# Kernel optimization log

Measured on AMD Instinct MI355X. Metric: run time of the kernel, lower is better.

## Reference

```python
import jax, jax.numpy as jnp
import numpy as np

B, T, D, H, C = 128, 1000, 40, 128, 8  # batch, time, input feats, hidden, classes


def _lstm_layer(x, Wih, Whh, bih, bhh):
    """Unidirectional LSTM over time. x: [B,T,Din] -> [B,T,H]. PyTorch gate order i,f,g,o."""
    Bn = x.shape[0]
    Hn = Whh.shape[1]
    b = bih + bhh
    def step(carry, xt):
        h, c = carry
        g = xt @ Wih.T + h @ Whh.T + b  # [B,4H]
        i, f, gg, o = jnp.split(g, 4, axis=-1)
        c = jax.nn.sigmoid(f) * c + jax.nn.sigmoid(i) * jnp.tanh(gg)
        h = jax.nn.sigmoid(o) * jnp.tanh(c)
        return (h, c), h
    h0 = jnp.zeros((Bn, Hn), x.dtype)
    _, hs = jax.lax.scan(step, (h0, h0), jnp.swapaxes(x, 0, 1))  # scan over time
    return jnp.swapaxes(hs, 0, 1)


def _bilstm_layer(x, pf, pb):
    fwd = _lstm_layer(x, *pf)
    bwd = jnp.flip(_lstm_layer(jnp.flip(x, 1), *pb), 1)
    return jnp.concatenate([fwd, bwd], axis=-1)  # [B,T,2H]


def setup_inputs() -> dict:
    key = jax.random.key(0)
    ks = jax.random.split(key, 16)
    s = 0.05
    def rn(k, shape):
        return jax.random.normal(k, shape, jnp.float32) * s
    inp = {"x": jax.random.normal(ks[0], (B, T, D), jnp.float32)}
    inp["ln_g"] = jnp.ones((D,), jnp.float32)
    inp["ln_b"] = jnp.zeros((D,), jnp.float32)
    dims = [D, 2 * H]  # layer-0 input feats, layer-1 input feats
    i = 1
    for l in range(2):
        for d in ("f", "b"):
            inp[f"Wih_{d}{l}"] = rn(ks[i], (4 * H, dims[l])); i += 1
            inp[f"Whh_{d}{l}"] = rn(ks[i], (4 * H, H)); i += 1
            inp[f"bih_{d}{l}"] = jnp.zeros((4 * H,), jnp.float32)
            inp[f"bhh_{d}{l}"] = jnp.zeros((4 * H,), jnp.float32)
    inp["attn_W1"] = rn(ks[i], (H, 2 * H)); i += 1
    inp["attn_b1"] = jnp.zeros((H,), jnp.float32)
    inp["attn_w2"] = rn(ks[i], (1, H)); i += 1
    inp["fc_W1"] = rn(ks[i], (H, 2 * H)); i += 1
    inp["fc_b1"] = jnp.zeros((H,), jnp.float32)
    inp["fc_W2"] = rn(ks[i], (C, H)); i += 1
    inp["fc_b2"] = jnp.zeros((C,), jnp.float32)
    return inp


def reference(x, ln_g, ln_b,
              Wih_f0, Whh_f0, bih_f0, bhh_f0, Wih_b0, Whh_b0, bih_b0, bhh_b0,
              Wih_f1, Whh_f1, bih_f1, bhh_f1, Wih_b1, Whh_b1, bih_b1, bhh_b1,
              attn_W1, attn_b1, attn_w2, fc_W1, fc_b1, fc_W2, fc_b2):
    # LayerNorm over feature dim (eps=1e-5, PyTorch default)
    mu = jnp.mean(x, axis=-1, keepdims=True)
    var = jnp.var(x, axis=-1, keepdims=True)
    xn = (x - mu) * jax.lax.rsqrt(var + 1e-5) * ln_g + ln_b
    # 2-layer bidirectional LSTM
    h = _bilstm_layer(xn, (Wih_f0, Whh_f0, bih_f0, bhh_f0), (Wih_b0, Whh_b0, bih_b0, bhh_b0))
    h = _bilstm_layer(h, (Wih_f1, Whh_f1, bih_f1, bhh_f1), (Wih_b1, Whh_b1, bih_b1, bhh_b1))
    # attention pooling: Linear-Tanh-Linear(no bias) -> softmax over time
    scores = jnp.tanh(h @ attn_W1.T + attn_b1) @ attn_w2[0]  # [B,T]
    w = jax.nn.softmax(scores, axis=1)
    ctx = jnp.einsum('bt,btd->bd', w, h)  # [B,2H]
    # MLP classifier head
    hid = jax.nn.relu(ctx @ fc_W1.T + fc_b1)
    return hid @ fc_W2.T + fc_b2  # [B,C] logits
```

## Files before the change

### kernel.cpp

```cpp
#include <hip/hip_runtime.h>
#include <hip/hip_fp16.h>

#define T_ 1000

typedef float v2f __attribute__((ext_vector_type(2)));
typedef __fp16 h2t __attribute__((ext_vector_type(2)));
typedef __fp16 h8v_t __attribute__((ext_vector_type(8)));

#if defined(__has_builtin)
#if __has_builtin(__builtin_amdgcn_fdot2)
#define HAS_FDOT2 1
#endif
#endif
#ifndef HAS_FDOT2
#define HAS_FDOT2 0
#endif

#define REC_BARRIER() asm volatile("s_waitcnt lgkmcnt(0)\n\ts_barrier" ::: "memory")

__device__ __forceinline__ float sigf(float x) { return 1.0f / (1.0f + __expf(-x)); }
__device__ __forceinline__ float tanh_fast(float x) { return 1.0f - 2.0f / (1.0f + __expf(2.0f * x)); }
__device__ __forceinline__ float dot4(float4 a, float4 b) {
  return a.x * b.x + a.y * b.y + a.z * b.z + a.w * b.w;
}
__device__ __forceinline__ void pkfma(v2f& acc, float4 w, float4 v) {
  v2f wl; wl[0] = w.x; wl[1] = w.y;
  v2f wh; wh[0] = w.z; wh[1] = w.w;
  v2f vl; vl[0] = v.x; vl[1] = v.y;
  v2f vh; vh[0] = v.z; vh[1] = v.w;
  acc += wl * vl;
  acc += wh * vh;
}
__device__ __forceinline__ unsigned short f2bf(float f) {
  unsigned u = __float_as_uint(f);
  u = (u + 0x7fffu + ((u >> 16) & 1u)) >> 16;
  return (unsigned short)u;
}
__device__ __forceinline__ float bf2f(unsigned short h) {
  return __uint_as_float(((unsigned)h) << 16);
}
__device__ __forceinline__ float4 bf4_to_f4(ushort4 u) {
  float4 r;
  r.x = bf2f(u.x); r.y = bf2f(u.y); r.z = bf2f(u.z); r.w = bf2f(u.w);
  return r;
}

__global__ void bail_kernel(float* out, int n) {
  for (int i = threadIdx.x; i < n; i += 256) out[i] = 0.0f;
}

__global__ __launch_bounds__(256) void ln_stats_kernel(const float* __restrict__ x,
                                                       float* __restrict__ mu_arr,
                                                       float* __restrict__ rs_arr) {
  const int lane = threadIdx.x & 63;
  const int w = threadIdx.x >> 6;
  const long row = (long)blockIdx.x * 4 + w;
  float v = (lane < 40) ? x[row * 40 + lane] : 0.0f;
  float s1 = v, s2 = v * v;
  for (int m = 32; m; m >>= 1) {
    s1 += __shfl_xor(s1, m, 64);
    s2 += __shfl_xor(s2, m, 64);
  }
  if (lane == 0) {
    const float mu = s1 * (1.0f / 40.0f);
    const float var = s2 * (1.0f / 40.0f) - mu * mu;
    mu_arr[row] = mu;
    rs_arr[row] = rsqrtf(var + 1e-5f);
  }
}

__global__ __launch_bounds__(256, 2) void gemm_xw0(
    const float* __restrict__ x,
    const float* __restrict__ mu_arr, const float* __restrict__ rs_arr,
    const float* __restrict__ ln_g, const float* __restrict__ ln_b,
    const float* __restrict__ Wf, const float* __restrict__ Wb,
    __fp16* __restrict__ xwf, __fp16* __restrict__ xwb,
    int Tc, int t0f, int t0b) {
  __shared__ float As[64 * 44];
  __shared__ float Bs[128 * 44];
  const int tid = threadIdx.x;
  const int tx = tid & 15, ty = tid >> 4;
  const int r0 = blockIdx.x * 64;
  const int jt = blockIdx.y;
  const int dir = jt >> 2, nh = jt & 3;
  const float* __restrict__ W = dir ? Wb : Wf;
  __fp16* __restrict__ out = dir ? xwb : xwf;
  const int jbase = nh * 128;
  const int t0 = dir ? t0b : t0f;

  float4* As4 = (float4*)As;
  float4* Bs4 = (float4*)Bs;
  {
    const int row = tid >> 2;
    const int t4 = tid & 3;
    const int r = r0 + row;
    const int br = r / Tc;
    const long xrow = (long)br * T_ + t0 + (r - br * Tc);
    const float mu = mu_arr[xrow];
    const float rs = rs_arr[xrow];
#pragma unroll
    for (int m = 0; m < 3; ++m) {
      const int k4 = t4 + m * 4;
      if (k4 < 10) {
        const float4 v = *(const float4*)&x[xrow * 40 + k4 * 4];
        const float4 g4 = *(const float4*)&ln_g[k4 * 4];
        const float4 b4 = *(const float4*)&ln_b[k4 * 4];
        float4 xn;
        xn.x = (v.x - mu) * rs * g4.x + b4.x;
        xn.y = (v.y - mu) * rs * g4.y + b4.y;
        xn.z = (v.z - mu) * rs * g4.z + b4.z;
        xn.w = (v.w - mu) * rs * g4.w + b4.w;
        As4[row * 11 + k4] = xn;
      }
    }
  }
  {
    const int row = tid & 127;
    const int h = tid >> 7;
#pragma unroll
    for (int m = 0; m < 5; ++m) {
      const int k4 = h + m * 2;
      Bs4[row * 11 + k4] = *(const float4*)&W[(long)(jbase + row) * 40 + k4 * 4];
    }
  }
  __syncthreads();

  v2f acc2[4][8];
#pragma unroll
  for (int r = 0; r < 4; ++r)
#pragma unroll
    for (int c2 = 0; c2 < 8; ++c2) acc2[r][c2] = 0.0f;
#pragma unroll 1
  for (int k4 = 0; k4 < 10; ++k4) {
    float4 av[4];
#pragma unroll
    for (int r = 0; r < 4; ++r) av[r] = As4[(ty * 4 + r) * 11 + k4];
#pragma unroll
    for (int c2 = 0; c2 < 8; ++c2) {
      const float4 bv = Bs4[(tx + 16 * c2) * 11 + k4];
#pragma unroll
      for (int r = 0; r < 4; ++r) pkfma(acc2[r][c2], av[r], bv);
    }
  }
#pragma unroll
  for (int r = 0; r < 4; ++r) {
    const long ob = (long)(r0 + ty * 4 + r) * 512 + jbase + tx;
#pragma unroll
    for (int c2 = 0; c2 < 8; ++c2) out[ob + c2 * 16] = (__fp16)(acc2[r][c2][0] + acc2[r][c2][1]);
  }
}

__global__ __launch_bounds__(512) void rec_fused(
    const __fp16* __restrict__ xw_f, const __fp16* __restrict__ xw_b,
    const float* __restrict__ Whh_f, const float* __restrict__ Whh_b,
    const float* __restrict__ bih_f, const float* __restrict__ bhh_f,
    const float* __restrict__ bih_b, const float* __restrict__ bhh_b,
    float* __restrict__ h0out, unsigned short* __restrict__ h1out, int out_bf16,
    float* __restrict__ state, int Tc, int t0f, int t0b, int first) {
  const int tid = threadIdx.x;
  const int u = (tid >> 6) * 16 + ((tid & 63) >> 2);
  const int p = tid & 3;
  const int brow = blockIdx.x & 127;
  const int dir = blockIdx.x >> 7;
  const __fp16* __restrict__ xw = dir ? xw_b : xw_f;
  const float* __restrict__ Whh = dir ? Whh_b : Whh_f;
  const float* __restrict__ bih = dir ? bih_b : bih_f;
  const float* __restrict__ bhh = dir ? bhh_b : bhh_f;
  const int t0 = dir ? t0b : t0f;

  h2t whp[4][16];
#pragma unroll
  for (int g = 0; g < 4; ++g) {
    const float4* wr4 = (const float4*)(Whh + (g * 128 + u) * 128);
#pragma unroll
    for (int ff = 0; ff < 4; ++ff) {
      const int c4 = (ff + p) & 3;
      const float4 wa = wr4[p * 8 + c4 * 2];
      const float4 wb = wr4[p * 8 + c4 * 2 + 1];
      h2t t0v; t0v[0] = (__fp16)wa.x; t0v[1] = (__fp16)wa.y;
      h2t t1v; t1v[0] = (__fp16)wa.z; t1v[1] = (__fp16)wa.w;
      h2t t2v; t2v[0] = (__fp16)wb.x; t2v[1] = (__fp16)wb.y;
      h2t t3v; t3v[0] = (__fp16)wb.z; t3v[1] = (__fp16)wb.w;
      whp[g][ff * 4 + 0] = t0v;
      whp[g][ff * 4 + 1] = t1v;
      whp[g][ff * 4 + 2] = t2v;
      whp[g][ff * 4 + 3] = t3v;
    }
  }
  const int myrow = p * 128 + u;
  const float bias_p = bih[myrow] + bhh[myrow];

  __shared__ h2t h16[2][64];
  __shared__ float hring[2][8][128];
  float* sblk = state + (long)blockIdx.x * 256;
  float c = 0.0f, hlast = 0.0f;
  if (first) {
    if (tid < 64) { h2t z; z[0] = (__fp16)0.0f; z[1] = (__fp16)0.0f; h16[0][tid] = z; }
  } else {
    if (tid < 64) {
      h2t pr; pr[0] = (__fp16)sblk[2 * tid]; pr[1] = (__fp16)sblk[2 * tid + 1];
      h16[0][tid] = pr;
    }
    c = sblk[128 + u];
  }
  const long gbase = (long)brow * Tc;
  float xr[8];
#pragma unroll
  for (int v = 0; v < 8; ++v) {
    xr[v] = 0.0f;
    if (v < Tc) {
      const int tr = dir ? (Tc - 1 - v) : v;
      xr[v] = (float)xw[(gbase + tr) * 512 + myrow];
    }
  }
  __syncthreads();

  const int nSB = (Tc + 7) / 8;
  const long obase = (long)brow * T_;
  for (int sb = 0; sb < nSB; ++sb) {
    const int rb = sb & 1;
#pragma unroll
    for (int su = 0; su < 8; ++su) {
      const int s = sb * 8 + su;
      if (s >= Tc) break;
      const int rdq = su & 1, wrq = rdq ^ 1;
      if (su == 0 && sb > 0) {
#pragma unroll
        for (int e = 0; e < 2; ++e) {
          const int idx = tid + e * 512;
          const int v = idx >> 7, j = idx & 127;
          const int s2 = (sb - 1) * 8 + v;
          const int tt = dir ? (Tc - 1 - s2) : s2;
          const long oidx = (obase + (t0 + tt)) * 256 + dir * 128 + j;
          const float hval = hring[rb ^ 1][v][j];
          if (out_bf16) h1out[oidx] = f2bf(hval);
          else          h0out[oidx] = hval;
        }
      }
      float a0 = 0.f, a1 = 0.f, a2 = 0.f, a3 = 0.f;
      const h8v_t* hp = (const h8v_t*)h16[rdq];
#pragma unroll
      for (int ff = 0; ff < 4; ++ff) {
        const int c4 = (ff + p) & 3;
        const h8v_t hx = hp[p * 4 + c4];
        const h2t x0 = __builtin_shufflevector(hx, hx, 0, 1);
        const h2t x1 = __builtin_shufflevector(hx, hx, 2, 3);
        const h2t x2 = __builtin_shufflevector(hx, hx, 4, 5);
        const h2t x3 = __builtin_shufflevector(hx, hx, 6, 7);
#if HAS_FDOT2
        a0 = __builtin_amdgcn_fdot2(x0, whp[0][ff * 4 + 0], a0, false);
        a0 = __builtin_amdgcn_fdot2(x1, whp[0][ff * 4 + 1], a0, false);
        a0 = __builtin_amdgcn_fdot2(x2, whp[0][ff * 4 + 2], a0, false);
        a0 = __builtin_amdgcn_fdot2(x3, whp[0][ff * 4 + 3], a0, false);
        a1 = __builtin_amdgcn_fdot2(x0, whp[1][ff * 4 + 0], a1, false);
        a1 = __builtin_amdgcn_fdot2(x1, whp[1][ff * 4 + 1], a1, false);
        a1 = __builtin_amdgcn_fdot2(x2, whp[1][ff * 4 + 2], a1, false);
        a1 = __builtin_amdgcn_fdot2(x3, whp[1][ff * 4 + 3], a1, false);
        a2 = __builtin_amdgcn_fdot2(x0, whp[2][ff * 4 + 0], a2, false);
        a2 = __builtin_amdgcn_fdot2(x1, whp[2][ff * 4 + 1], a2, false);
        a2 = __builtin_amdgcn_fdot2(x2, whp[2][ff * 4 + 2], a2, false);
        a2 = __builtin_amdgcn_fdot2(x3, whp[2][ff * 4 + 3], a2, false);
        a3 = __builtin_amdgcn_fdot2(x0, whp[3][ff * 4 + 0], a3, false);
        a3 = __builtin_amdgcn_fdot2(x1, whp[3][ff * 4 + 1], a3, false);
        a3 = __builtin_amdgcn_fdot2(x2, whp[3][ff * 4 + 2], a3, false);
        a3 = __builtin_amdgcn_fdot2(x3, whp[3][ff * 4 + 3], a3, false);
#else
        const h2t xs[4] = {x0, x1, x2, x3};
#pragma unroll
        for (int j = 0; j < 4; ++j) {
          a0 = fmaf((float)xs[j][0], (float)whp[0][ff * 4 + j][0], a0);
          a0 = fmaf((float)xs[j][1], (float)whp[0][ff * 4 + j][1], a0);
          a1 = fmaf((float)xs[j][0], (float)whp[1][ff * 4 + j][0], a1);
          a1 = fmaf((float)xs[j][1], (float)whp[1][ff * 4 + j][1], a1);
          a2 = fmaf((float)xs[j][0], (float)whp[2][ff * 4 + j][0], a2);
          a2 = fmaf((float)xs[j][1], (float)whp[2][ff * 4 + j][1], a2);
          a3 = fmaf((float)xs[j][0], (float)whp[3][ff * 4 + j][0], a3);
          a3 = fmaf((float)xs[j][1], (float)whp[3][ff * 4 + j][1], a3);
        }
#endif
      }
      const float xin = xr[su] + bias_p;
      float pg0 = a0 + ((p == 0) ? xin : 0.0f);
      float pg1 = a1 + ((p == 1) ? xin : 0.0f);
      float pg2 = a2 + ((p == 2) ? xin : 0.0f);
      float pg3 = a3 + ((p == 3) ? xin : 0.0f);
      pg0 += __shfl_xor(pg0, 1, 64); pg0 += __shfl_xor(pg0, 2, 64);
      pg1 += __shfl_xor(pg1, 1, 64); pg1 += __shfl_xor(pg1, 2, 64);
      pg2 += __shfl_xor(pg2, 1, 64); pg2 += __shfl_xor(pg2, 2, 64);
      pg3 += __shfl_xor(pg3, 1, 64); pg3 += __shfl_xor(pg3, 2, 64);
      const float ig = sigf(pg0);
      const float fg = sigf(pg1);
      const float gg = tanh_fast(pg2);
      const float og = sigf(pg3);
      c = fg * c + ig * gg;
      const float hv2 = og * tanh_fast(c);
      if (p == 0) {
        ((__fp16*)h16[wrq])[u] = (__fp16)hv2;
        hring[rb][su][u] = hv2;
        hlast = hv2;
      }
      if (su == 7) {
#pragma unroll
        for (int v = 0; v < 8; ++v) {
          const int sn = s + 1 + v;
          xr[v] = 0.0f;
          if (sn < Tc) {
            const int tr = dir ? (Tc - 1 - sn) : sn;
            xr[v] = (float)xw[(gbase + tr) * 512 + myrow];
          }
        }
      }
      REC_BARRIER();
    }
  }
  {
    const int sbL = (Tc - 1) >> 3;
    const int cnt = Tc - sbL * 8;
    const int rbL = sbL & 1;
#pragma unroll
    for (int e = 0; e < 2; ++e) {
      const int idx = tid + e * 512;
      const int v = idx >> 7, j = idx & 127;
      if (v < cnt) {
        const int s2 = sbL * 8 + v;
        const int tt = dir ? (Tc - 1 - s2) : s2;
        const long oidx = (obase + (t0 + tt)) * 256 + dir * 128 + j;
        const float hval = hring[rbL][v][j];
        if (out_bf16) h1out[oidx] = f2bf(hval);
        else          h0out[oidx] = hval;
      }
    }
  }
  if (p == 0) { sblk[u] = hlast; sblk[128 + u] = c; }
}

__global__ __launch_bounds__(256, 2) void gemm_xw1(
    const float* __restrict__ h0,
    const float* __restrict__ Wf, const float* __restrict__ Wb,
    __fp16* __restrict__ xwf, __fp16* __restrict__ xwb,
    int Tc, int t0f, int t0b) {
  __shared__ float As[64 * 36];
  __shared__ float Bs[128 * 36];
  __shared__ int rowbase[64];
  const int tid = threadIdx.x;
  const int tx = tid & 15, ty = tid >> 4;
  const int r0 = blockIdx.x * 64;
  const int jt = blockIdx.y;
  const int dir = jt >> 2;
  const int nh = jt & 3;
  const float* __restrict__ W = dir ? Wb : Wf;
  __fp16* __restrict__ out = dir ? xwb : xwf;
  const int jbase = nh * 128;
  const int t0 = dir ? t0b : t0f;

  if (tid < 64) {
    const int r = r0 + tid;
    const int br = r / Tc;
    rowbase[tid] = br * T_ + t0 + (r - br * Tc);
  }

  float4* As4 = (float4*)As;
  float4* Bs4 = (float4*)Bs;
  v2f acc2[4][8];
#pragma unroll
  for (int r = 0; r < 4; ++r)
#pragma unroll
    for (int c2 = 0; c2 < 8; ++c2) acc2[r][c2] = 0.0f;
#pragma unroll 1
  for (int kk = 0; kk < 8; ++kk) {
    __syncthreads();
#pragma unroll
    for (int i = 0; i < 2; ++i) {
      const int q = tid + i * 256;
      const int row = q >> 3, k4 = q & 7;
      As4[row * 9 + k4] = *(const float4*)&h0[(long)rowbase[row] * 256 + kk * 32 + k4 * 4];
    }
#pragma unroll
    for (int i = 0; i < 4; ++i) {
      const int q = tid + i * 256;
      const int row = q >> 3, k4 = q & 7;
      Bs4[row * 9 + k4] = *(const float4*)&W[(long)(jbase + row) * 256 + kk * 32 + k4 * 4];
    }
    __syncthreads();
#pragma unroll 1
    for (int k4 = 0; k4 < 8; ++k4) {
      float4 av[4];
#pragma unroll
      for (int r = 0; r < 4; ++r) av[r] = As4[(ty * 4 + r) * 9 + k4];
#pragma unroll
      for (int c2 = 0; c2 < 8; ++c2) {
        const float4 bv = Bs4[(tx + 16 * c2) * 9 + k4];
#pragma unroll
        for (int r = 0; r < 4; ++r) pkfma(acc2[r][c2], av[r], bv);
      }
    }
  }
#pragma unroll
  for (int r = 0; r < 4; ++r) {
    const long ob = (long)(r0 + ty * 4 + r) * 512 + jbase + tx;
#pragma unroll
    for (int c2 = 0; c2 < 8; ++c2) out[ob + c2 * 16] = (__fp16)(acc2[r][c2][0] + acc2[r][c2][1]);
  }
}

__global__ __launch_bounds__(256, 2) void score_kernel(
    const unsigned short* __restrict__ h1b, const float* __restrict__ W1,
    const float* __restrict__ b1, const float* __restrict__ w2,
    float* __restrict__ scores) {
  __shared__ float As[64 * 36];
  __shared__ float Bs[128 * 36];
  const int tid = threadIdx.x;
  const int tx = tid & 15, ty = tid >> 4;
  const long r0 = (long)blockIdx.x * 64;

  float4* As4 = (float4*)As;
  float4* Bs4 = (float4*)Bs;
  v2f acc2[4][8];
#pragma unroll
  for (int r = 0; r < 4; ++r)
#pragma unroll
    for (int c2 = 0; c2 < 8; ++c2) acc2[r][c2] = 0.0f;
#pragma unroll 1
  for (int kk = 0; kk < 8; ++kk) {
    __syncthreads();
#pragma unroll
    for (int i = 0; i < 2; ++i) {
      const int q = tid + i * 256;
      const int row = q >> 3, k4 = q & 7;
      const ushort4 uv = *(const ushort4*)&h1b[(r0 + row) * 256 + kk * 32 + k4 * 4];
      As4[row * 9 + k4] = bf4_to_f4(uv);
    }
#pragma unroll
    for (int i = 0; i < 4; ++i) {
      const int q = tid + i * 256;
      const int row = q >> 3, k4 = q & 7;
      Bs4[row * 9 + k4] = *(const float4*)&W1[(long)row * 256 + kk * 32 + k4 * 4];
    }
    __syncthreads();
#pragma unroll 1
    for (int k4 = 0; k4 < 8; ++k4) {
      float4 av[4];
#pragma unroll
      for (int r = 0; r < 4; ++r) av[r] = As4[(ty * 4 + r) * 9 + k4];
#pragma unroll
      for (int c2 = 0; c2 < 8; ++c2) {
        const float4 bv = Bs4[(tx + 16 * c2) * 9 + k4];
#pragma unroll
        for (int r = 0; r < 4; ++r) pkfma(acc2[r][c2], av[r], bv);
      }
    }
  }
#pragma unroll
  for (int r = 0; r < 4; ++r) {
    float s = 0.0f;
#pragma unroll
    for (int c2 = 0; c2 < 8; ++c2) {
      const int col = tx + 16 * c2;
      s += tanh_fast(acc2[r][c2][0] + acc2[r][c2][1] + b1[col]) * w2[col];
    }
#pragma unroll
    for (int m = 1; m < 16; m <<= 1) s += __shfl_xor(s, m, 16);
    if (tx == 0) scores[r0 + ty * 4 + r] = s;
  }
}

__global__ __launch_bounds__(256, 2) void head_kernel(
    const float* __restrict__ scores, const unsigned short* __restrict__ h1b,
    const float* __restrict__ fW1, const float* __restrict__ fb1,
    const float* __restrict__ fW2, const float* __restrict__ fb2,
    float* __restrict__ outp) {
  const int b = blockIdx.x, tid = threadIdx.x;
  __shared__ float wls[1000];
  __shared__ float red[8];
  __shared__ __align__(16) float ctx[256];
  __shared__ __align__(16) float hid[128];

  float sv[4];
  float mx = -1e30f;
#pragma unroll
  for (int i = 0; i < 4; ++i) {
    const int t = tid + i * 256;
    sv[i] = (t < 1000) ? scores[b * 1000 + t] : -1e30f;
    mx = fmaxf(mx, sv[i]);
  }
  for (int m = 32; m; m >>= 1) mx = fmaxf(mx, __shfl_xor(mx, m, 64));
  if ((tid & 63) == 0) red[tid >> 6] = mx;
  __syncthreads();
  mx = fmaxf(fmaxf(red[0], red[1]), fmaxf(red[2], red[3]));
  float se = 0.0f;
#pragma unroll
  for (int i = 0; i < 4; ++i) {
    const int t = tid + i * 256;
    if (t < 1000) {
      const float e = __expf(sv[i] - mx);
      wls[t] = e;
      se += e;
    }
  }
  for (int m = 32; m; m >>= 1) se += __shfl_xor(se, m, 64);
  if ((tid & 63) == 0) red[4 + (tid >> 6)] = se;
  __syncthreads();
  const float rinv = 1.0f / (red[4] + red[5] + red[6] + red[7]);

  float a = 0.0f;
  const unsigned short* hb = h1b + (long)b * T_ * 256 + tid;
  for (int t = 0; t < T_; ++t) a = fmaf(wls[t], bf2f(hb[t * 256]), a);
  ctx[tid] = a * rinv;
  __syncthreads();
  if (tid < 128) {
    float s = fb1[tid];
    const float4* wr = (const float4*)&fW1[tid * 256];
    const float4* cc = (const float4*)ctx;
#pragma unroll
    for (int f = 0; f < 64; ++f) s += dot4(wr[f], cc[f]);
    hid[tid] = fmaxf(s, 0.0f);
  }
  __syncthreads();
  if (tid < 8) {
    float s = fb2[tid];
    const float4* wr = (const float4*)&fW2[tid * 128];
    const float4* hh = (const float4*)hid;
#pragma unroll
    for (int f = 0; f < 32; ++f) s += dot4(wr[f], hh[f]);
    outp[b * 8 + tid] = s;
  }
}

extern "C" void kernel_launch(void* const* d_in, const int* in_sizes, int n_in,
                              void* d_out, int out_size, void* d_ws, size_t ws_size,
                              hipStream_t stream) {
  (void)in_sizes; (void)n_in; (void)out_size;
  const float* x       = (const float*)d_in[0];
  const float* ln_g    = (const float*)d_in[1];
  const float* ln_b    = (const float*)d_in[2];
  const float* Wih_f0  = (const float*)d_in[3];
  const float* Whh_f0  = (const float*)d_in[4];
  const float* bih_f0  = (const float*)d_in[5];
  const float* bhh_f0  = (const float*)d_in[6];
  const float* Wih_b0  = (const float*)d_in[7];
  const float* Whh_b0  = (const float*)d_in[8];
  const float* bih_b0  = (const float*)d_in[9];
  const float* bhh_b0  = (const float*)d_in[10];
  const float* Wih_f1  = (const float*)d_in[11];
  const float* Whh_f1  = (const float*)d_in[12];
  const float* bih_f1  = (const float*)d_in[13];
  const float* bhh_f1  = (const float*)d_in[14];
  const float* Wih_b1  = (const float*)d_in[15];
  const float* Whh_b1  = (const float*)d_in[16];
  const float* bih_b1  = (const float*)d_in[17];
  const float* bhh_b1  = (const float*)d_in[18];
  const float* attn_W1 = (const float*)d_in[19];
  const float* attn_b1 = (const float*)d_in[20];
  const float* attn_w2 = (const float*)d_in[21];
  const float* fc_W1   = (const float*)d_in[22];
  const float* fc_b1   = (const float*)d_in[23];
  const float* fc_W2   = (const float*)d_in[24];
  const float* fc_b2   = (const float*)d_in[25];

  char* base = (char*)d_ws;
  size_t off = 0;
  auto alloc = [&](size_t bytes) {
    char* ptr = base + off;
    off += (bytes + 255) & ~(size_t)255;
    return ptr;
  };
  float*          h0    = (float*)alloc(32768000ull * 4);
  unsigned short* h1b   = (unsigned short*)alloc(32768000ull * 2);
  float*          state = (float*)alloc(65536ull * 4);
  float*          scor  = (float*)alloc(128000ull * 4);
  float*          mu_a  = (float*)alloc(128000ull * 4);
  float*          rs_a  = (float*)alloc(128000ull * 4);

  const size_t rem = (ws_size > off) ? (ws_size - off) : 0;
  static const int cands[16] = {1000, 500, 250, 200, 125, 100, 50, 40, 25, 20, 10, 8, 5, 4, 2, 1};
  int Tc = 0;
  for (int ci = 0; ci < 16; ++ci) {
    if (262144ull * (size_t)cands[ci] <= rem) { Tc = cands[ci]; break; }
  }
  if (Tc == 0) {
    bail_kernel<<<dim3(1), dim3(256), 0, stream>>>((float*)d_out, 1024);
    return;
  }
  __fp16* xwf = (__fp16*)(base + off);
  __fp16* xwb = xwf + 65536L * Tc;

  ln_stats_kernel<<<dim3(32000), dim3(256), 0, stream>>>(x, mu_a, rs_a);
  const int nch = T_ / Tc;
  for (int ch = 0; ch < nch; ++ch) {
    const int t0f = ch * Tc;
    const int t0b = T_ - (ch + 1) * Tc;
    gemm_xw0<<<dim3(2 * Tc, 8), dim3(256), 0, stream>>>(x, mu_a, rs_a, ln_g, ln_b,
                                                        Wih_f0, Wih_b0, xwf, xwb, Tc, t0f, t0b);
    rec_fused<<<dim3(256), dim3(512), 0, stream>>>(xwf, xwb, Whh_f0, Whh_b0,
                                                   bih_f0, bhh_f0, bih_b0, bhh_b0,
                                                   h0, h1b, 0, state, Tc, t0f, t0b,
                                                   (ch == 0) ? 1 : 0);
  }
  for (int ch = 0; ch < nch; ++ch) {
    const int t0f = ch * Tc;
    const int t0b = T_ - (ch + 1) * Tc;
    gemm_xw1<<<dim3(2 * Tc, 8), dim3(256), 0, stream>>>(h0, Wih_f1, Wih_b1, xwf, xwb, Tc, t0f, t0b);
    rec_fused<<<dim3(256), dim3(512), 0, stream>>>(xwf, xwb, Whh_f1, Whh_b1,
                                                   bih_f1, bhh_f1, bih_b1, bhh_b1,
                                                   h0, h1b, 1, state, Tc, t0f, t0b,
                                                   (ch == 0) ? 1 : 0);
  }
  score_kernel<<<dim3(2000), dim3(256), 0, stream>>>(h1b, attn_W1, attn_b1, attn_w2, scor);
  head_kernel<<<dim3(128), dim3(256), 0, stream>>>(scor, h1b, fc_W1, fc_b1, fc_W2, fc_b2,
                                                   (float*)d_out);
}
```

Baseline: 3.380 ms.

## Batch 8 rows per block and compute recurrent matvec with MFMA

```diff
diff --git a/kernel.cpp b/kernel.cpp
--- a/kernel.cpp
+++ b/kernel.cpp
@@ -6,15 +6,7 @@
 typedef float v2f __attribute__((ext_vector_type(2)));
 typedef __fp16 h2t __attribute__((ext_vector_type(2)));
 typedef __fp16 h8v_t __attribute__((ext_vector_type(8)));
-
-#if defined(__has_builtin)
-#if __has_builtin(__builtin_amdgcn_fdot2)
-#define HAS_FDOT2 1
-#endif
-#endif
-#ifndef HAS_FDOT2
-#define HAS_FDOT2 0
-#endif
+typedef float f32x4 __attribute__((ext_vector_type(4)));
 
 #define REC_BARRIER() asm volatile("s_waitcnt lgkmcnt(0)\n\ts_barrier" ::: "memory")
 
@@ -150,7 +142,7 @@
   }
 }
 
-__global__ __launch_bounds__(512) void rec_fused(
+__global__ __launch_bounds__(512) void rec_mfma(
     const __fp16* __restrict__ xw_f, const __fp16* __restrict__ xw_b,
     const float* __restrict__ Whh_f, const float* __restrict__ Whh_b,
     const float* __restrict__ bih_f, const float* __restrict__ bhh_f,
@@ -158,180 +150,130 @@
     float* __restrict__ h0out, unsigned short* __restrict__ h1out, int out_bf16,
     float* __restrict__ state, int Tc, int t0f, int t0b, int first) {
   const int tid = threadIdx.x;
-  const int u = (tid >> 6) * 16 + ((tid & 63) >> 2);
-  const int p = tid & 3;
-  const int brow = blockIdx.x & 127;
-  const int dir = blockIdx.x >> 7;
+  const int w = tid >> 6;
+  const int l = tid & 63;
+  const int al = l & 15;
+  const int kg = l >> 4;
+  const int dir = blockIdx.x & 1;
+  const int bg = blockIdx.x >> 1;
+  const int brow0 = bg * 8;
   const __fp16* __restrict__ xw = dir ? xw_b : xw_f;
   const float* __restrict__ Whh = dir ? Whh_b : Whh_f;
   const float* __restrict__ bih = dir ? bih_b : bih_f;
   const float* __restrict__ bhh = dir ? bhh_b : bhh_f;
   const int t0 = dir ? t0b : t0f;
 
-  h2t whp[4][16];
-#pragma unroll
-  for (int g = 0; g < 4; ++g) {
-    const float4* wr4 = (const float4*)(Whh + (g * 128 + u) * 128);
-#pragma unroll
-    for (int ff = 0; ff < 4; ++ff) {
-      const int c4 = (ff + p) & 3;
-      const float4 wa = wr4[p * 8 + c4 * 2];
-      const float4 wb = wr4[p * 8 + c4 * 2 + 1];
-      h2t t0v; t0v[0] = (__fp16)wa.x; t0v[1] = (__fp16)wa.y;
-      h2t t1v; t1v[0] = (__fp16)wa.z; t1v[1] = (__fp16)wa.w;
-      h2t t2v; t2v[0] = (__fp16)wb.x; t2v[1] = (__fp16)wb.y;
-      h2t t3v; t3v[0] = (__fp16)wb.z; t3v[1] = (__fp16)wb.w;
-      whp[g][ff * 4 + 0] = t0v;
-      whp[g][ff * 4 + 1] = t1v;
-      whp[g][ff * 4 + 2] = t2v;
-      whp[g][ff * 4 + 3] = t3v;
-    }
-  }
-  const int myrow = p * 128 + u;
-  const float bias_p = bih[myrow] + bhh[myrow];
-
-  __shared__ h2t h16[2][64];
-  __shared__ float hring[2][8][128];
-  float* sblk = state + (long)blockIdx.x * 256;
-  float c = 0.0f, hlast = 0.0f;
-  if (first) {
-    if (tid < 64) { h2t z; z[0] = (__fp16)0.0f; z[1] = (__fp16)0.0f; h16[0][tid] = z; }
-  } else {
-    if (tid < 64) {
-      h2t pr; pr[0] = (__fp16)sblk[2 * tid]; pr[1] = (__fp16)sblk[2 * tid + 1];
-      h16[0][tid] = pr;
-    }
-    c = sblk[128 + u];
-  }
-  const long gbase = (long)brow * Tc;
-  float xr[8];
-#pragma unroll
-  for (int v = 0; v < 8; ++v) {
-    xr[v] = 0.0f;
-    if (v < Tc) {
-      const int tr = dir ? (Tc - 1 - v) : v;
-      xr[v] = (float)xw[(gbase + tr) * 512 + myrow];
-    }
-  }
-  __syncthreads();
-
-  const int nSB = (Tc + 7) / 8;
-  const long obase = (long)brow * T_;
-  for (int sb = 0; sb < nSB; ++sb) {
-    const int rb = sb & 1;
-#pragma unroll
-    for (int su = 0; su < 8; ++su) {
-      const int s = sb * 8 + su;
-      if (s >= Tc) break;
-      const int rdq = su & 1, wrq = rdq ^ 1;
-      if (su == 0 && sb > 0) {
-#pragma unroll
-        for (int e = 0; e < 2; ++e) {
-          const int idx = tid + e * 512;
-          const int v = idx >> 7, j = idx & 127;
-          const int s2 = (sb - 1) * 8 + v;
-          const int tt = dir ? (Tc - 1 - s2) : s2;
-          const long oidx = (obase + (t0 + tt)) * 256 + dir * 128 + j;
-          const float hval = hring[rb ^ 1][v][j];
-          if (out_bf16) h1out[oidx] = f2bf(hval);
-          else          h0out[oidx] = hval;
-        }
+  h8v_t wA[4][4];
+#pragma unroll
+  for (int mt = 0; mt < 4; ++mt) {
+    const int grow = w * 64 + mt * 16 + al;
+#pragma unroll
+    for (int kt = 0; kt < 4; ++kt) {
+      const int k0 = kt * 32 + kg * 8;
+      const float4 wa = *(const float4*)&Whh[(long)grow * 128 + k0];
+      const float4 wb = *(const float4*)&Whh[(long)grow * 128 + k0 + 4];
+      h8v_t v;
+      v[0] = (__fp16)wa.x; v[1] = (__fp16)wa.y; v[2] = (__fp16)wa.z; v[3] = (__fp16)wa.w;
+      v[4] = (__fp16)wb.x; v[5] = (__fp16)wb.y; v[6] = (__fp16)wb.z; v[7] = (__fp16)wb.w;
+      wA[mt][kt] = v;
+    }
+  }
+  const int u2 = tid & 127;
+  const int q = tid >> 7;
+  float bsum[4];
+#pragma unroll
+  for (int g = 0; g < 4; ++g) bsum[g] = bih[g * 128 + u2] + bhh[g * 128 + u2];
+
+  __shared__ __align__(16) __fp16 h16[2][16][136];
+  __shared__ float gacc[512][9];
+
+  float* sblk = state + (long)blockIdx.x * 2048;
+  for (int i = tid; i < 2 * 16 * 136; i += 512) ((__fp16*)h16)[i] = (__fp16)0.0f;
+  float cc0 = 0.0f, cc1 = 0.0f;
+  __syncthreads();
+  if (!first) {
+    for (int i = tid; i < 1024; i += 512) {
+      const int b = i >> 7, uu = i & 127;
+      h16[0][b][(((uu >> 5) + b) & 3) * 32 + (uu & 31)] = (__fp16)sblk[i];
+    }
+    cc0 = sblk[1024 + (2 * q) * 128 + u2];
+    cc1 = sblk[1024 + (2 * q + 1) * 128 + u2];
+  }
+  float xwreg[8];
+  {
+    const int tr0 = dir ? (Tc - 1) : 0;
+#pragma unroll
+    for (int g = 0; g < 4; ++g)
+#pragma unroll
+      for (int j = 0; j < 2; ++j) {
+        const int b = 2 * q + j;
+        xwreg[g * 2 + j] = (float)xw[((long)(brow0 + b) * Tc + tr0) * 512 + g * 128 + u2];
       }
-      float a0 = 0.f, a1 = 0.f, a2 = 0.f, a3 = 0.f;
-      const h8v_t* hp = (const h8v_t*)h16[rdq];
-#pragma unroll
-      for (int ff = 0; ff < 4; ++ff) {
-        const int c4 = (ff + p) & 3;
-        const h8v_t hx = hp[p * 4 + c4];
-        const h2t x0 = __builtin_shufflevector(hx, hx, 0, 1);
-        const h2t x1 = __builtin_shufflevector(hx, hx, 2, 3);
-        const h2t x2 = __builtin_shufflevector(hx, hx, 4, 5);
-        const h2t x3 = __builtin_shufflevector(hx, hx, 6, 7);
-#if HAS_FDOT2
-        a0 = __builtin_amdgcn_fdot2(x0, whp[0][ff * 4 + 0], a0, false);
-        a0 = __builtin_amdgcn_fdot2(x1, whp[0][ff * 4 + 1], a0, false);
-        a0 = __builtin_amdgcn_fdot2(x2, whp[0][ff * 4 + 2], a0, false);
-        a0 = __builtin_amdgcn_fdot2(x3, whp[0][ff * 4 + 3], a0, false);
-        a1 = __builtin_amdgcn_fdot2(x0, whp[1][ff * 4 + 0], a1, false);
-        a1 = __builtin_amdgcn_fdot2(x1, whp[1][ff * 4 + 1], a1, false);
-        a1 = __builtin_amdgcn_fdot2(x2, whp[1][ff * 4 + 2], a1, false);
-        a1 = __builtin_amdgcn_fdot2(x3, whp[1][ff * 4 + 3], a1, false);
-        a2 = __builtin_amdgcn_fdot2(x0, whp[2][ff * 4 + 0], a2, false);
-        a2 = __builtin_amdgcn_fdot2(x1, whp[2][ff * 4 + 1], a2, false);
-        a2 = __builtin_amdgcn_fdot2(x2, whp[2][ff * 4 + 2], a2, false);
-        a2 = __builtin_amdgcn_fdot2(x3, whp[2][ff * 4 + 3], a2, false);
-        a3 = __builtin_amdgcn_fdot2(x0, whp[3][ff * 4 + 0], a3, false);
-        a3 = __builtin_amdgcn_fdot2(x1, whp[3][ff * 4 + 1], a3, false);
-        a3 = __builtin_amdgcn_fdot2(x2, whp[3][ff * 4 + 2], a3, false);
-        a3 = __builtin_amdgcn_fdot2(x3, whp[3][ff * 4 + 3], a3, false);
-#else
-        const h2t xs[4] = {x0, x1, x2, x3};
-#pragma unroll
-        for (int j = 0; j < 4; ++j) {
-          a0 = fmaf((float)xs[j][0], (float)whp[0][ff * 4 + j][0], a0);
-          a0 = fmaf((float)xs[j][1], (float)whp[0][ff * 4 + j][1], a0);
-          a1 = fmaf((float)xs[j][0], (float)whp[1][ff * 4 + j][0], a1);
-          a1 = fmaf((float)xs[j][1], (float)whp[1][ff * 4 + j][1], a1);
-          a2 = fmaf((float)xs[j][0], (float)whp[2][ff * 4 + j][0], a2);
-          a2 = fmaf((float)xs[j][1], (float)whp[2][ff * 4 + j][1], a2);
-          a3 = fmaf((float)xs[j][0], (float)whp[3][ff * 4 + j][0], a3);
-          a3 = fmaf((float)xs[j][1], (float)whp[3][ff * 4 + j][1], a3);
-        }
-#endif
+  }
+  __syncthreads();
+
+  for (int s = 0; s < Tc; ++s) {
+    const int rq = s & 1, wq = rq ^ 1;
+    h8v_t Bf[4];
+#pragma unroll
+    for (int kt = 0; kt < 4; ++kt)
+      Bf[kt] = *(const h8v_t*)&h16[rq][al][(((kt + al) & 3) << 5) + (kg << 3)];
+#pragma unroll
+    for (int mt = 0; mt < 4; ++mt) {
+      f32x4 acc = {0.0f, 0.0f, 0.0f, 0.0f};
+#pragma unroll
+      for (int kt = 0; kt < 4; ++kt)
+        acc = __builtin_amdgcn_mfma_f32_16x16x32_f16(wA[mt][kt], Bf[kt], acc, 0, 0, 0);
+      if (al < 8) {
+#pragma unroll
+        for (int r = 0; r < 4; ++r)
+          gacc[w * 64 + mt * 16 + kg * 4 + r][al] = acc[r];
       }
-      const float xin = xr[su] + bias_p;
-      float pg0 = a0 + ((p == 0) ? xin : 0.0f);
-      float pg1 = a1 + ((p == 1) ? xin : 0.0f);
-      float pg2 = a2 + ((p == 2) ? xin : 0.0f);
-      float pg3 = a3 + ((p == 3) ? xin : 0.0f);
-      pg0 += __shfl_xor(pg0, 1, 64); pg0 += __shfl_xor(pg0, 2, 64);
-      pg1 += __shfl_xor(pg1, 1, 64); pg1 += __shfl_xor(pg1, 2, 64);
-      pg2 += __shfl_xor(pg2, 1, 64); pg2 += __shfl_xor(pg2, 2, 64);
-      pg3 += __shfl_xor(pg3, 1, 64); pg3 += __shfl_xor(pg3, 2, 64);
-      const float ig = sigf(pg0);
-      const float fg = sigf(pg1);
-      const float gg = tanh_fast(pg2);
-      const float og = sigf(pg3);
-      c = fg * c + ig * gg;
-      const float hv2 = og * tanh_fast(c);
-      if (p == 0) {
-        ((__fp16*)h16[wrq])[u] = (__fp16)hv2;
-        hring[rb][su][u] = hv2;
-        hlast = hv2;
+    }
+    REC_BARRIER();
+    const int tglob = t0 + (dir ? (Tc - 1 - s) : s);
+#pragma unroll
+    for (int j = 0; j < 2; ++j) {
+      const int b = 2 * q + j;
+      const float gi = gacc[u2][b]       + xwreg[0 * 2 + j] + bsum[0];
+      const float gf = gacc[128 + u2][b] + xwreg[1 * 2 + j] + bsum[1];
+      const float gg = gacc[256 + u2][b] + xwreg[2 * 2 + j] + bsum[2];
+      const float go = gacc[384 + u2][b] + xwreg[3 * 2 + j] + bsum[3];
+      const float ig = sigf(gi);
+      const float fg = sigf(gf);
+      const float g2 = tanh_fast(gg);
+      const float og = sigf(go);
+      float c = j ? cc1 : cc0;
+      c = fg * c + ig * g2;
+      if (j) cc1 = c; else cc0 = c;
+      const float hv = og * tanh_fast(c);
+      h16[wq][b][(((u2 >> 5) + b) & 3) * 32 + (u2 & 31)] = (__fp16)hv;
+      const long oidx = ((long)(brow0 + b) * T_ + tglob) * 256 + dir * 128 + u2;
+      if (out_bf16) h1out[oidx] = f2bf(hv);
+      else          h0out[oidx] = hv;
+    }
+    {
+      const int sn = s + 1;
+      if (sn < Tc) {
+        const int tr = dir ? (Tc - 1 - sn) : sn;
+#pragma unroll
+        for (int g = 0; g < 4; ++g)
+#pragma unroll
+          for (int j = 0; j < 2; ++j) {
+            const int b = 2 * q + j;
+            xwreg[g * 2 + j] = (float)xw[((long)(brow0 + b) * Tc + tr) * 512 + g * 128 + u2];
+          }
       }
-      if (su == 7) {
-#pragma unroll
-        for (int v = 0; v < 8; ++v) {
-          const int sn = s + 1 + v;
-          xr[v] = 0.0f;
-          if (sn < Tc) {
-            const int tr = dir ? (Tc - 1 - sn) : sn;
-            xr[v] = (float)xw[(gbase + tr) * 512 + myrow];
-          }
-        }
-      }
-      REC_BARRIER();
-    }
-  }
-  {
-    const int sbL = (Tc - 1) >> 3;
-    const int cnt = Tc - sbL * 8;
-    const int rbL = sbL & 1;
-#pragma unroll
-    for (int e = 0; e < 2; ++e) {
-      const int idx = tid + e * 512;
-      const int v = idx >> 7, j = idx & 127;
-      if (v < cnt) {
-        const int s2 = sbL * 8 + v;
-        const int tt = dir ? (Tc - 1 - s2) : s2;
-        const long oidx = (obase + (t0 + tt)) * 256 + dir * 128 + j;
-        const float hval = hring[rbL][v][j];
-        if (out_bf16) h1out[oidx] = f2bf(hval);
-        else          h0out[oidx] = hval;
-      }
-    }
-  }
-  if (p == 0) { sblk[u] = hlast; sblk[128 + u] = c; }
+    }
+    REC_BARRIER();
+  }
+  const int fin = Tc & 1;
+  for (int i = tid; i < 1024; i += 512) {
+    const int b = i >> 7, uu = i & 127;
+    sblk[i] = (float)h16[fin][b][(((uu >> 5) + b) & 3) * 32 + (uu & 31)];
+  }
+  sblk[1024 + (2 * q) * 128 + u2] = cc0;
+  sblk[1024 + (2 * q + 1) * 128 + u2] = cc1;
 }
 
 __global__ __launch_bounds__(256, 2) void gemm_xw1(
@@ -591,19 +533,19 @@
     const int t0b = T_ - (ch + 1) * Tc;
     gemm_xw0<<<dim3(2 * Tc, 8), dim3(256), 0, stream>>>(x, mu_a, rs_a, ln_g, ln_b,
                                                         Wih_f0, Wih_b0, xwf, xwb, Tc, t0f, t0b);
-    rec_fused<<<dim3(256), dim3(512), 0, stream>>>(xwf, xwb, Whh_f0, Whh_b0,
-                                                   bih_f0, bhh_f0, bih_b0, bhh_b0,
-                                                   h0, h1b, 0, state, Tc, t0f, t0b,
-                                                   (ch == 0) ? 1 : 0);
+    rec_mfma<<<dim3(32), dim3(512), 0, stream>>>(xwf, xwb, Whh_f0, Whh_b0,
+                                                 bih_f0, bhh_f0, bih_b0, bhh_b0,
+                                                 h0, h1b, 0, state, Tc, t0f, t0b,
+                                                 (ch == 0) ? 1 : 0);
   }
   for (int ch = 0; ch < nch; ++ch) {
     const int t0f = ch * Tc;
     const int t0b = T_ - (ch + 1) * Tc;
     gemm_xw1<<<dim3(2 * Tc, 8), dim3(256), 0, stream>>>(h0, Wih_f1, Wih_b1, xwf, xwb, Tc, t0f, t0b);
-    rec_fused<<<dim3(256), dim3(512), 0, stream>>>(xwf, xwb, Whh_f1, Whh_b1,
-                                                   bih_f1, bhh_f1, bih_b1, bhh_b1,
-                                                   h0, h1b, 1, state, Tc, t0f, t0b,
-                                                   (ch == 0) ? 1 : 0);
+    rec_mfma<<<dim3(32), dim3(512), 0, stream>>>(xwf, xwb, Whh_f1, Whh_b1,
+                                                 bih_f1, bhh_f1, bih_b1, bhh_b1,
+                                                 h0, h1b, 1, state, Tc, t0f, t0b,
+                                                 (ch == 0) ? 1 : 0);
   }
   score_kernel<<<dim3(2000), dim3(256), 0, stream>>>(h1b, attn_W1, attn_b1, attn_w2, scor);
   head_kernel<<<dim3(128), dim3(256), 0, stream>>>(scor, h1b, fc_W1, fc_b1, fc_W2, fc_b2,
```

After: 4.554 ms. 1.35x slower.
